# Optimization experiments

Measured on AMD Instinct MI355X. Metric: run time of the kernel, lower is better.

The kernel has to match this reference:

```python
import jax, jax.numpy as jnp
import numpy as np

B, N, DIM = 2, 1024, 1024   # seq_len must equal dim (dots contracts q's feature dim with kkt's n_y dim)
HEADS, DIM_HEAD = 16, 64    # heads * dim_head == dim (required by residual + LayerNorm(dim))
SCALE = DIM_HEAD ** -0.5
EPS = 1e-5


def setup_inputs() -> dict:
    key = jax.random.key(0)
    ks = jax.random.split(key, 7)
    w = 1.0 / np.sqrt(DIM)  # kaiming-ish linear init keeps logits sane
    return {
        "x": jax.random.normal(ks[0], (B, N, DIM), dtype=jnp.float32),
        "y": jax.random.normal(ks[1], (B, N, DIM), dtype=jnp.float32),
        "Wq": jax.random.normal(ks[2], (DIM, DIM), dtype=jnp.float32) * w,
        "Wk": jax.random.normal(ks[3], (DIM, HEADS * DIM_HEAD), dtype=jnp.float32) * w,
        "Wv": jax.random.normal(ks[4], (DIM, HEADS * DIM_HEAD), dtype=jnp.float32) * w,
        "gamma": jnp.ones((DIM,), dtype=jnp.float32),
        "beta": jnp.zeros((DIM,), dtype=jnp.float32),
    }


def _layer_norm(z, gamma, beta):
    m = jnp.mean(z, axis=-1, keepdims=True)
    v = jnp.mean(jnp.square(z - m), axis=-1, keepdims=True)
    return (z - m) * jax.lax.rsqrt(v + EPS) * gamma + beta


def reference(x, y, Wq, Wk, Wv, gamma, beta):
    b, n, _ = y.shape
    q = x @ Wq                                                     # (b, n, dim); shared across heads (torch repeats)
    k = (y @ Wk).reshape(b, n, HEADS, DIM_HEAD).transpose(0, 2, 1, 3)  # (b, h, n, dh)
    v = (y @ Wv).reshape(b, n, HEADS, DIM_HEAD).transpose(0, 2, 1, 3)  # (b, h, n, dh)
    kkt = jnp.einsum('bhid,bhjd->bhij', k, k) * SCALE              # (b, h, n, n)
    dots = jnp.einsum('bid,bhjd->bhij', q, kkt) * SCALE            # contract q's dim (== n) with kkt rows
    attn = jax.nn.softmax(dots, axis=-1)
    out = jnp.einsum('bhij,bhjd->bhid', attn, v)                   # (b, h, n, dh)
    out = out.transpose(0, 2, 1, 3).reshape(b, n, HEADS * DIM_HEAD)
    return _layer_norm(out + y, gamma, beta)
```

## Files before the change

kernel.cpp:

```cpp
#include <hip/hip_runtime.h>

#define NB 2
#define NN 1024
#define ND 1024
#define NH 16
#define SCALE2 0.015625f
#define SCL2E 0.022542182f
#define DEFER_THR 11.0f
#define LNEPS 1e-5f
#define NSPLIT 2
#define JPS (16 / NSPLIT)

typedef _Float16 f16x8 __attribute__((ext_vector_type(8)));
typedef _Float16 f16x4 __attribute__((ext_vector_type(4)));
typedef float f32x4 __attribute__((ext_vector_type(4)));


__device__ inline void gload_lds16(const void* g, void* l) {
    __builtin_amdgcn_global_load_lds(
        (const __attribute__((address_space(1))) void*)g,
        (__attribute__((address_space(3))) void*)l, 16, 0, 0);
}

__device__ inline f32x4 vmax4(f32x4 a, f32x4 b) {
    f32x4 c;
    c[0] = fmaxf(a[0], b[0]); c[1] = fmaxf(a[1], b[1]);
    c[2] = fmaxf(a[2], b[2]); c[3] = fmaxf(a[3], b[3]);
    return c;
}

__global__ __launch_bounds__(256) void prep(const float* __restrict__ x,
                                            const float* __restrict__ y,
                                            const float* __restrict__ Wq,
                                            const float* __restrict__ Wk,
                                            const float* __restrict__ Wv,
                                            _Float16* __restrict__ xh,
                                            _Float16* __restrict__ yh,
                                            _Float16* __restrict__ WqT,
                                            _Float16* __restrict__ WkT,
                                            _Float16* __restrict__ WvT) {
    __shared__ float tile[32][33];
    const int bid = blockIdx.x;
    const int tid = threadIdx.x;
    if (bid < 2048) {
        const float* src = (bid < 1024) ? x : y;
        _Float16* dst = (bid < 1024) ? xh : yh;
        int base = (bid & 1023) * 2048 + tid * 8;
        f32x4 a = *(const f32x4*)&src[base];
        f32x4 c = *(const f32x4*)&src[base + 4];
        *(f16x4*)&dst[base] = __builtin_convertvector(a, f16x4);
        *(f16x4*)&dst[base + 4] = __builtin_convertvector(c, f16x4);
    } else {
        int seg = (bid - 2048) >> 10;
        int t = (bid - 2048) & 1023;
        const float* src = seg == 0 ? Wq : seg == 1 ? Wk : Wv;
        _Float16* dst = seg == 0 ? WqT : seg == 1 ? WkT : WvT;
        int tx = tid & 31, ty = tid >> 5;
        int c0 = (t & 31) * 32, r0 = (t >> 5) * 32;
#pragma unroll
        for (int i = 0; i < 4; ++i)
            tile[ty + 8 * i][tx] = src[(size_t)(r0 + ty + 8 * i) * 1024 + c0 + tx];
        __syncthreads();
#pragma unroll
        for (int i = 0; i < 4; ++i)
            dst[(size_t)(c0 + ty + 8 * i) * 1024 + r0 + tx] = (_Float16)tile[tx][ty + 8 * i];
    }
}

template <int BM, int BN>
__device__ __forceinline__ void gemm_body(const _Float16* __restrict__ A,
                                          const _Float16* __restrict__ BT,
                                          int lda, int ldb,
                                          int brow, int bcol, int K,
                                          int mode, _Float16* __restrict__ out0,
                                          _Float16* __restrict__ out1,
                                          int ldc, int zoff) {
    __shared__ _Float16 Asm[2][2][BM * 32];
    __shared__ _Float16 Bsm[2][2][BN * 32];
    constexpr int MR = BM / 32;
    constexpr int NC = BN / 32;
    constexpr int APASS = BM * 32 * 2 / 4096;
    constexpr int BPASS = BN * 32 * 2 / 4096;
    static_assert(BM * 32 * 2 % 4096 == 0 && BN * 32 * 2 % 4096 == 0, "pass alignment");
    static_assert(2 * (APASS + BPASS) == 6, "vmcnt(6) assumes 6 loads per stage");

    const int tid = threadIdx.x;
    const int lane = tid & 63;
    const int w = tid >> 6;
    const int wr = w >> 1, wc = w & 1;
    const int g = lane >> 4, r = lane & 15;

    f32x4 acc[MR][NC];
#pragma unroll
    for (int m = 0; m < MR; ++m)
#pragma unroll
        for (int n = 0; n < NC; ++n) acc[m][n] = (f32x4){0.f, 0.f, 0.f, 0.f};

    auto stage = [&](int buf, int kof) {
#pragma unroll
        for (int s = 0; s < 2; ++s) {
#pragma unroll
            for (int p = 0; p < APASS; ++p) {
                int o = (p * 256 + tid) * 16;
                int row = o >> 6, cb = o & 63;
                gload_lds16((const char*)(A + (size_t)(brow + row) * lda + kof + s * 32) + cb,
                            (char*)Asm[buf][s] + o);
            }
#pragma unroll
            for (int p = 0; p < BPASS; ++p) {
                int o = (p * 256 + tid) * 16;
                int row = o >> 6, cb = o & 63;
                gload_lds16((const char*)(BT + (size_t)(bcol + row) * ldb + kof + s * 32) + cb,
                            (char*)Bsm[buf][s] + o);
            }
        }
    };

    stage(0, 0);

    int buf = 0;
    const int nk = K / 64;
    for (int kt = 0; kt < nk; ++kt) {
        if (kt + 1 < nk) {
            stage(buf ^ 1, (kt + 1) * 64);
            asm volatile("s_waitcnt vmcnt(6)" ::: "memory");
        } else {
            asm volatile("s_waitcnt vmcnt(0)" ::: "memory");
        }
        __builtin_amdgcn_s_barrier();

#pragma unroll
        for (int s = 0; s < 2; ++s) {
            f16x8 af[MR], bf[NC];
#pragma unroll
            for (int m = 0; m < MR; ++m)
                af[m] = *(const f16x8*)&Asm[buf][s][((BM / 2) * wr + 16 * m + r) * 32 + 8 * g];
#pragma unroll
            for (int n = 0; n < NC; ++n)
                bf[n] = *(const f16x8*)&Bsm[buf][s][((BN / 2) * wc + 16 * n + r) * 32 + 8 * g];
#pragma unroll
            for (int m = 0; m < MR; ++m)
#pragma unroll
                for (int n = 0; n < NC; ++n)
                    acc[m][n] = __builtin_amdgcn_mfma_f32_16x16x32_f16(af[m], bf[n], acc[m][n], 0, 0, 0);
        }
        __builtin_amdgcn_s_barrier();
        buf ^= 1;
    }

#pragma unroll
    for (int m = 0; m < MR; ++m)
#pragma unroll
        for (int n = 0; n < NC; ++n) {
            const int colg = bcol + (BN / 2) * wc + 16 * n + r;
            const int rowbase = brow + (BM / 2) * wr + 16 * m + 4 * g;
            if (mode == 0) {
#pragma unroll
                for (int r4 = 0; r4 < 4; ++r4)
                    out0[(size_t)(rowbase + r4) * ldc + colg] = (_Float16)acc[m][n][r4];
            } else if (mode == 1) {
                f16x4 pk = __builtin_convertvector(acc[m][n], f16x4);
                *(f16x4*)&out1[(size_t)colg * 2048 + rowbase] = pk;
                int hh = colg >> 6, dh = colg & 63;
#pragma unroll
                for (int r4 = 0; r4 < 4; ++r4) {
                    int kv = rowbase + r4;
                    int bb = kv >> 10, kvl = kv & 1023;
                    size_t flat = (((size_t)((bb * 16 + hh) * 64 + (kvl >> 4)) * 2 + (dh >> 5)) << 9)
                                  + (((kvl & 15) * 4 + ((dh >> 3) & 3)) << 3) + (dh & 7);
                    out0[flat] = pk[r4];
                }
            } else if (mode == 3) {
                int hh = rowbase >> 6, mpart_ = (rowbase >> 4) & 3;
                int bb = colg >> 10, kvl = colg & 1023;
#pragma unroll
                for (int r4 = 0; r4 < 4; ++r4) {
                    int dsub = (rowbase & 63) + r4;
                    size_t flat = (((size_t)((((bb * 16 + hh) * 4 + mpart_) * 16 + (kvl >> 6)) * 2
                                             + ((kvl >> 5) & 1))) << 9)
                                  + (((dsub & 15) * 4 + ((kvl >> 3) & 3)) << 3) + (kvl & 7);
                    out0[flat] = (_Float16)acc[m][n][r4];
                }
            } else {
                int hh = colg >> 6, dh = colg & 63;
#pragma unroll
                for (int r4 = 0; r4 < 4; ++r4) {
                    int row = rowbase + r4;
                    size_t flat = (((size_t)((zoff * 16 + hh) * 64 + (row >> 4)) * 2 + (dh >> 5)) << 9)
                                  + (((row & 15) * 4 + ((dh >> 3) & 3)) << 3) + (dh & 7);
                    out0[flat] = (_Float16)(acc[m][n][r4] * SCL2E);
                }
            }
        }
}

__global__ __launch_bounds__(256) void gemm_a(const _Float16* __restrict__ xh,
                                              const _Float16* __restrict__ yh,
                                              const _Float16* __restrict__ WqT,
                                              const _Float16* __restrict__ WkT,
                                              _Float16* __restrict__ qh,
                                              _Float16* __restrict__ kfrag,
                                              _Float16* __restrict__ kT) {
    const int bid = blockIdx.x;
    const int t = bid & 255;
    if (bid < 256)
        gemm_body<128, 64>(xh, WqT, 1024, 1024, (t >> 4) * 128, (t & 15) * 64, 1024,
                           0, qh, nullptr, 1024, 0);
    else
        gemm_body<128, 64>(yh, WkT, 1024, 1024, (t >> 4) * 128, (t & 15) * 64, 1024,
                           1, kfrag, kT, 0, 0);
}

__global__ __launch_bounds__(256) void gemm_b(const _Float16* __restrict__ qh,
                                              const _Float16* __restrict__ kT,
                                              const _Float16* __restrict__ yh,
                                              const _Float16* __restrict__ WvT,
                                              _Float16* __restrict__ qfrag,
                                              _Float16* __restrict__ vfrag) {
    const int bid = blockIdx.x;
    if (bid < 256) {
        int z = bid >> 7, t = bid & 127;
        gemm_body<128, 64>(qh + (size_t)z * NN * ND, kT + z * NN, 1024, 2048,
                           (t >> 4) * 128, (t & 15) * 64, 1024, 4, qfrag, nullptr, 0, z);
    } else {
        int t = bid - 256;
        gemm_body<128, 64>(WvT, yh, 1024, 1024, (t >> 5) * 128, (t & 31) * 64, 1024,
                           3, vfrag, nullptr, 0, 0);
    }
}

__global__ __launch_bounds__(256) void flash_part(const _Float16* __restrict__ Qfrag,
                                                  const _Float16* __restrict__ Kfrag,
                                                  const _Float16* __restrict__ Vfrag,
                                                  _Float16* __restrict__ opart,
                                                  float* __restrict__ mpart,
                                                  float* __restrict__ lpart) {
    __shared__ _Float16 Ks[2][4096];
    __shared__ _Float16 Vs[2][4096];
    __shared__ _Float16 Ps[4][2][16][72];
    const int it = blockIdx.x;
    const int bh = blockIdx.y;
    const int sp = blockIdx.z;
    const int b = bh >> 4, h = bh & 15;

    const int tid = threadIdx.x;
    const int lane = tid & 63;
    const int w = tid >> 6;
    const int g = lane >> 4, r = lane & 15;
    const int ch8 = ((r << 2) + g) << 3;

    const _Float16* Kf = Kfrag + ((size_t)bh << 16);
    const _Float16* Vf = Vfrag + ((size_t)bh << 16);

    auto stageKV = [&](int buf, int jt) {
#pragma unroll
        for (int q = 0; q < 2; ++q) {
            int c = q * 4 + w;
            gload_lds16(&Kf[jt * 4096 + c * 512 + lane * 8], &Ks[buf][c * 512 + lane * 8]);
        }
#pragma unroll
        for (int q = 0; q < 2; ++q) {
            int c = q * 4 + w;
            int n = c >> 1, half = c & 1;
            gload_lds16(&Vf[(n * 16 + jt) * 1024 + half * 512 + lane * 8],
                        &Vs[buf][n * 1024 + half * 512 + lane * 8]);
        }
    };

    f16x8 qa[2][2];
#pragma unroll
    for (int u = 0; u < 2; ++u)
#pragma unroll
        for (int kk = 0; kk < 2; ++kk)
            qa[u][kk] = *(const f16x8*)
                &Qfrag[((((size_t)bh * 64 + it * 8 + w * 2 + u) * 2 + kk) << 9) + ch8];

    float m_i[2] = {-1e30f, -1e30f}, l_i[2] = {0.f, 0.f};
    f32x4 o[2][4];
#pragma unroll
    for (int u = 0; u < 2; ++u)
#pragma unroll
        for (int n = 0; n < 4; ++n) o[u][n] = (f32x4){0.f, 0.f, 0.f, 0.f};

    const int jt0 = sp * JPS;
    stageKV(0, jt0);

    int buf = 0;
    for (int j = 0; j < JPS; ++j) {
        if (j + 1 < JPS) {
            stageKV(buf ^ 1, jt0 + j + 1);
            asm volatile("s_waitcnt vmcnt(4)" ::: "memory");
        } else {
            asm volatile("s_waitcnt vmcnt(0)" ::: "memory");
        }
        __builtin_amdgcn_s_barrier();

        f16x8 kfr[4][2];
#pragma unroll
        for (int f = 0; f < 4; ++f)
#pragma unroll
            for (int kk = 0; kk < 2; ++kk)
                kfr[f][kk] = *(const f16x8*)&Ks[buf][(f * 2 + kk) * 512 + ch8];

        f32x4 sT[2][4];
#pragma unroll
        for (int u = 0; u < 2; ++u)
#pragma unroll
            for (int f = 0; f < 4; ++f) sT[u][f] = (f32x4){0.f, 0.f, 0.f, 0.f};
#pragma unroll
        for (int f = 0; f < 4; ++f)
#pragma unroll
            for (int kk = 0; kk < 2; ++kk)
#pragma unroll
                for (int u = 0; u < 2; ++u)
                    sT[u][f] = __builtin_amdgcn_mfma_f32_16x16x32_f16(kfr[f][kk], qa[u][kk], sT[u][f], 0, 0, 0);

        f16x8 vfr[4][2];
#pragma unroll
        for (int n = 0; n < 4; ++n)
#pragma unroll
            for (int kk = 0; kk < 2; ++kk)
                vfr[n][kk] = *(const f16x8*)&Vs[buf][n * 1024 + kk * 512 + ch8];

#pragma unroll
        for (int u = 0; u < 2; ++u) {
            f32x4 mm = vmax4(vmax4(sT[u][0], sT[u][1]), vmax4(sT[u][2], sT[u][3]));
            float mx = fmaxf(fmaxf(mm[0], mm[1]), fmaxf(mm[2], mm[3]));
            mx = fmaxf(mx, __shfl_xor(mx, 16));
            mx = fmaxf(mx, __shfl_xor(mx, 32));
            if (!__all(mx <= m_i[u] + DEFER_THR)) {
                float mnew = fmaxf(m_i[u], mx);
                float corr = exp2f(m_i[u] - mnew);
                m_i[u] = mnew;
                l_i[u] *= corr;
#pragma unroll
                for (int n = 0; n < 4; ++n) o[u][n] *= corr;
            }
            f32x4 p[4];
#pragma unroll
            for (int f = 0; f < 4; ++f)
#pragma unroll
                for (int reg = 0; reg < 4; ++reg)
                    p[f][reg] = exp2f(sT[u][f][reg] - m_i[u]);
            f32x4 ps4 = (p[0] + p[1]) + (p[2] + p[3]);
            float rs = (ps4[0] + ps4[1]) + (ps4[2] + ps4[3]);
            rs += __shfl_xor(rs, 16);
            rs += __shfl_xor(rs, 32);
            l_i[u] += rs;
#pragma unroll
            for (int f = 0; f < 4; ++f)
                *(f16x4*)&Ps[w][u][r][16 * f + 4 * g] = __builtin_convertvector(p[f], f16x4);
        }

        f16x8 pa[2][2];
#pragma unroll
        for (int u = 0; u < 2; ++u)
#pragma unroll
            for (int kk = 0; kk < 2; ++kk)
                pa[u][kk] = *(const f16x8*)&Ps[w][u][r][kk * 32 + 8 * g];

#pragma unroll
        for (int n = 0; n < 4; ++n)
#pragma unroll
            for (int kk = 0; kk < 2; ++kk)
#pragma unroll
                for (int u = 0; u < 2; ++u)
                    o[u][n] = __builtin_amdgcn_mfma_f32_16x16x32_f16(vfr[n][kk], pa[u][kk], o[u][n], 0, 0, 0);

        __builtin_amdgcn_s_barrier();
        buf ^= 1;
    }

    _Float16* Ob = opart + (size_t)sp * NB * NN * ND
                   + ((size_t)b * NN + it * 128 + 32 * w) * ND + h * 64;
#pragma unroll
    for (int u = 0; u < 2; ++u) {
        float inv = 1.0f / l_i[u];
#pragma unroll
        for (int n = 0; n < 4; ++n)
            *(f16x4*)&Ob[(size_t)(u * 16 + r) * ND + 16 * n + 4 * g] =
                __builtin_convertvector(o[u][n] * inv, f16x4);
    }
    if (lane < 16) {
        int base = (((sp * NB) + b) * NH + h) * NN + it * 128 + 32 * w + r;
        mpart[base] = m_i[0];
        lpart[base] = l_i[0];
        mpart[base + 16] = m_i[1];
        lpart[base + 16] = l_i[1];
    }
}

__global__ __launch_bounds__(256) void ln_combine(const _Float16* __restrict__ opart,
                                                  const float* __restrict__ mpart,
                                                  const float* __restrict__ lpart,
                                                  const float* __restrict__ Y,
                                                  const float* __restrict__ gamma,
                                                  const float* __restrict__ beta,
                                                  float* __restrict__ Out) {
    const int row = blockIdx.x;
    const int b = row >> 10, n = row & 1023;
    const int t = threadIdx.x;
    const int c0 = t * 4;
    const int h = c0 >> 6;

    float ms[NSPLIT], ls[NSPLIT];
    float M = -1e30f;
#pragma unroll
    for (int s = 0; s < NSPLIT; ++s) {
        int idx = (((s * NB) + b) * NH + h) * NN + n;
        ms[s] = mpart[idx];
        ls[s] = lpart[idx];
        M = fmaxf(M, ms[s]);
    }
    float wsum = 0.f;
    f32x4 acc = (f32x4){0.f, 0.f, 0.f, 0.f};
#pragma unroll
    for (int s = 0; s < NSPLIT; ++s) {
        float wgt = exp2f(ms[s] - M) * ls[s];
        wsum += wgt;
        f16x4 ov = *(const f16x4*)&opart[(size_t)s * NB * NN * ND + (size_t)row * ND + c0];
        acc += wgt * __builtin_convertvector(ov, f32x4);
    }
    f32x4 z = acc * (1.0f / wsum) + *(const f32x4*)&Y[(size_t)row * ND + c0];

    __shared__ float red[8];
    float s1 = z.x + z.y + z.z + z.w;
#pragma unroll
    for (int off = 32; off; off >>= 1) s1 += __shfl_xor(s1, off);
    if ((t & 63) == 0) red[t >> 6] = s1;
    __syncthreads();
    float mean = (red[0] + red[1] + red[2] + red[3]) * (1.0f / 1024.0f);

    f32x4 d = z - mean;
    float sq = d.x * d.x + d.y * d.y + d.z * d.z + d.w * d.w;
#pragma unroll
    for (int off = 32; off; off >>= 1) sq += __shfl_xor(sq, off);
    if ((t & 63) == 0) red[4 + (t >> 6)] = sq;
    __syncthreads();
    float var = (red[4] + red[5] + red[6] + red[7]) * (1.0f / 1024.0f);
    float rstd = rsqrtf(var + LNEPS);

    f32x4 gg = *(const f32x4*)&gamma[c0];
    f32x4 bb = *(const f32x4*)&beta[c0];
    f32x4 res = d * rstd * gg + bb;
    *(f32x4*)&Out[(size_t)row * ND + c0] = res;
}

extern "C" void kernel_launch(void* const* d_in, const int* in_sizes, int n_in,
                              void* d_out, int out_size, void* d_ws, size_t ws_size,
                              hipStream_t stream) {
    const float* x = (const float*)d_in[0];
    const float* y = (const float*)d_in[1];
    const float* Wq = (const float*)d_in[2];
    const float* Wk = (const float*)d_in[3];
    const float* Wv = (const float*)d_in[4];
    const float* gamma = (const float*)d_in[5];
    const float* beta = (const float*)d_in[6];
    float* out = (float*)d_out;

    const size_t MB = 1024ull * 1024ull;
    char* w = (char*)d_ws;
    _Float16* xh    = (_Float16*)(w + 0 * MB);
    _Float16* yh    = (_Float16*)(w + 4 * MB);
    _Float16* WqT   = (_Float16*)(w + 8 * MB);
    _Float16* WkT   = (_Float16*)(w + 10 * MB);
    _Float16* WvT   = (_Float16*)(w + 12 * MB);
    _Float16* qh    = (_Float16*)(w + 14 * MB);
    _Float16* kT    = (_Float16*)(w + 18 * MB);
    _Float16* kfrag = (_Float16*)(w + 22 * MB);
    _Float16* vfrag = (_Float16*)(w + 26 * MB);
    _Float16* qfrag = (_Float16*)(w + 30 * MB);
    _Float16* opart = (_Float16*)(w + 34 * MB);
    float* mpart = (float*)(w + 42 * MB);
    float* lpart = (float*)(w + 43 * MB);

    prep<<<5120, 256, 0, stream>>>(x, y, Wq, Wk, Wv, xh, yh, WqT, WkT, WvT);

    gemm_a<<<512, 256, 0, stream>>>(xh, yh, WqT, WkT, qh, kfrag, kT);

    gemm_b<<<512, 256, 0, stream>>>(qh, kT, yh, WvT, qfrag, vfrag);

    flash_part<<<dim3(8, 32, NSPLIT), 256, 0, stream>>>(qfrag, kfrag, vfrag, opart, mpart, lpart);

    ln_combine<<<NB * NN, 256, 0, stream>>>(opart, mpart, lpart, y, gamma, beta, out);
}
```

Baseline: 77.97 us.

## Rebalance GEMM stages: fold V projection into QKV kernel, split-K the q·kkt GEMM

The V projection moves from the second GEMM launch into the first, so the first launch covers Q, K and V (768 blocks) with a 3-blocks-per-CU launch bound. The q·kT GEMM now splits its K dimension into two halves across 512 blocks, writing two fp16 partial qfrag buffers. The flash kernel sums the two halves when it loads Q fragments. The intent is to balance work between the two GEMM launches and fill the GPU better. The cost is extra qfrag memory traffic and fp16 rounding of the partial sums.

```diff
diff --git a/kernel.cpp b/kernel.cpp
--- a/kernel.cpp
+++ b/kernel.cpp
@@ -194,39 +194,43 @@
         }
 }
 
-__global__ __launch_bounds__(256) void gemm_a(const _Float16* __restrict__ xh,
-                                              const _Float16* __restrict__ yh,
-                                              const _Float16* __restrict__ WqT,
-                                              const _Float16* __restrict__ WkT,
-                                              _Float16* __restrict__ qh,
-                                              _Float16* __restrict__ kfrag,
-                                              _Float16* __restrict__ kT) {
+__global__ __launch_bounds__(256, 3) void gemm_qkv(const _Float16* __restrict__ xh,
+                                                   const _Float16* __restrict__ yh,
+                                                   const _Float16* __restrict__ WqT,
+                                                   const _Float16* __restrict__ WkT,
+                                                   const _Float16* __restrict__ WvT,
+                                                   _Float16* __restrict__ qh,
+                                                   _Float16* __restrict__ kfrag,
+                                                   _Float16* __restrict__ kT,
+                                                   _Float16* __restrict__ vfrag) {
     const int bid = blockIdx.x;
-    const int t = bid & 255;
-    if (bid < 256)
+    if (bid < 256) {
+        int t = bid;
         gemm_body<128, 64>(xh, WqT, 1024, 1024, (t >> 4) * 128, (t & 15) * 64, 1024,
                            0, qh, nullptr, 1024, 0);
-    else
+    } else if (bid < 512) {
+        int t = bid - 256;
         gemm_body<128, 64>(yh, WkT, 1024, 1024, (t >> 4) * 128, (t & 15) * 64, 1024,
                            1, kfrag, kT, 0, 0);
-}
-
-__global__ __launch_bounds__(256) void gemm_b(const _Float16* __restrict__ qh,
-                                              const _Float16* __restrict__ kT,
-                                              const _Float16* __restrict__ yh,
-                                              const _Float16* __restrict__ WvT,
-                                              _Float16* __restrict__ qfrag,
-                                              _Float16* __restrict__ vfrag) {
-    const int bid = blockIdx.x;
-    if (bid < 256) {
-        int z = bid >> 7, t = bid & 127;
-        gemm_body<128, 64>(qh + (size_t)z * NN * ND, kT + z * NN, 1024, 2048,
-                           (t >> 4) * 128, (t & 15) * 64, 1024, 4, qfrag, nullptr, 0, z);
     } else {
-        int t = bid - 256;
+        int t = bid - 512;
         gemm_body<128, 64>(WvT, yh, 1024, 1024, (t >> 5) * 128, (t & 31) * 64, 1024,
                            3, vfrag, nullptr, 0, 0);
     }
+}
+
+__global__ __launch_bounds__(256) void gemm_qk(const _Float16* __restrict__ qh,
+                                               const _Float16* __restrict__ kT,
+                                               _Float16* __restrict__ qfrag) {
+    const int bid = blockIdx.x;
+    const int t = bid & 127;
+    const int zh = bid >> 7;
+    const int z = zh >> 1, half = zh & 1;
+    const size_t QHALF = (size_t)NB * NN * ND;
+    gemm_body<128, 64>(qh + (size_t)z * NN * ND + half * 512,
+                       kT + z * NN + half * 512,
+                       1024, 2048, (t >> 4) * 128, (t & 15) * 64, 512,
+                       4, qfrag + (size_t)half * QHALF, nullptr, 0, z);
 }
 
 __global__ __launch_bounds__(256) void flash_part(const _Float16* __restrict__ Qfrag,
@@ -251,6 +255,7 @@
 
     const _Float16* Kf = Kfrag + ((size_t)bh << 16);
     const _Float16* Vf = Vfrag + ((size_t)bh << 16);
+    const size_t QHALF = (size_t)NB * NN * ND;
 
     auto stageKV = [&](int buf, int jt) {
 #pragma unroll
@@ -271,9 +276,12 @@
 #pragma unroll
     for (int u = 0; u < 2; ++u)
 #pragma unroll
-        for (int kk = 0; kk < 2; ++kk)
-            qa[u][kk] = *(const f16x8*)
-                &Qfrag[((((size_t)bh * 64 + it * 8 + w * 2 + u) * 2 + kk) << 9) + ch8];
+        for (int kk = 0; kk < 2; ++kk) {
+            size_t qidx = ((((size_t)bh * 64 + it * 8 + w * 2 + u) * 2 + kk) << 9) + ch8;
+            f16x8 a0 = *(const f16x8*)&Qfrag[qidx];
+            f16x8 a1 = *(const f16x8*)&Qfrag[QHALF + qidx];
+            qa[u][kk] = a0 + a1;
+        }
 
     float m_i[2] = {-1e30f, -1e30f}, l_i[2] = {0.f, 0.f};
     f32x4 o[2][4];
@@ -470,15 +478,15 @@
     _Float16* kfrag = (_Float16*)(w + 22 * MB);
     _Float16* vfrag = (_Float16*)(w + 26 * MB);
     _Float16* qfrag = (_Float16*)(w + 30 * MB);
-    _Float16* opart = (_Float16*)(w + 34 * MB);
-    float* mpart = (float*)(w + 42 * MB);
-    float* lpart = (float*)(w + 43 * MB);
+    _Float16* opart = (_Float16*)(w + 38 * MB);
+    float* mpart = (float*)(w + 46 * MB);
+    float* lpart = (float*)(w + 47 * MB);
 
     prep<<<5120, 256, 0, stream>>>(x, y, Wq, Wk, Wv, xh, yh, WqT, WkT, WvT);
 
-    gemm_a<<<512, 256, 0, stream>>>(xh, yh, WqT, WkT, qh, kfrag, kT);
-
-    gemm_b<<<512, 256, 0, stream>>>(qh, kT, yh, WvT, qfrag, vfrag);
+    gemm_qkv<<<768, 256, 0, stream>>>(xh, yh, WqT, WkT, WvT, qh, kfrag, kT, vfrag);
+
+    gemm_qk<<<512, 256, 0, stream>>>(qh, kT, qfrag);
 
     flash_part<<<dim3(8, 32, NSPLIT), 256, 0, stream>>>(qfrag, kfrag, vfrag, opart, mpart, lpart);
 
```

Result: slower. 80.47 us (+3.2%).
